# Optimization experiments

Measured on AMD Instinct MI355X. Metric: run time of the kernel, lower is better.

## Reference

```python
import jax
import jax.numpy as jnp
from jax import lax
import numpy as np

B, T, IN, H, K = 8, 4096, 512, 512, 2


def setup_inputs() -> dict:
    key = jax.random.key(0)
    k = jax.random.split(key, 5)
    scale_w0 = 1.0 / np.sqrt(IN * K)
    scale_w1 = 1.0 / np.sqrt(H * K)
    return {
        "x": jax.random.normal(k[0], (B, T, IN), jnp.float32),
        "w0": jax.random.normal(k[1], (3 * H, IN, K), jnp.float32) * scale_w0,
        "b0": jax.random.normal(k[2], (3 * H,), jnp.float32) * scale_w0,
        "w1": jax.random.normal(k[3], (3 * H, H, K), jnp.float32) * scale_w1,
        "b1": jax.random.normal(k[4], (3 * H,), jnp.float32) * scale_w1,
    }


def _qrnn_layer(x, w, b):
    # x: [B, T, C]; w: [3H, C, K]; causal conv (left pad K-1), matching
    # torch padding=K-1 then slicing off the last K-1 timesteps.
    xc = jnp.transpose(x, (0, 2, 1))  # [B, C, T]
    conv = lax.conv_general_dilated(
        xc, w, window_strides=(1,), padding=[(K - 1, 0)],
        dimension_numbers=("NCH", "OIH", "NCH"))
    conv = conv + b[None, :, None]
    conv = jnp.transpose(conv, (0, 2, 1))  # [B, T, 3H]
    z, f, o = jnp.split(conv, 3, axis=-1)
    z = jnp.tanh(z)
    f = jax.nn.sigmoid(f)
    o = jax.nn.sigmoid(o)

    def step(h, zfo):
        zt, ft, ot = zfo
        h = ft * h + (1.0 - ft) * zt  # fo-pool recurrence
        return h, ot * h

    h0 = jnp.zeros((x.shape[0], z.shape[-1]), x.dtype)
    hT, outs = lax.scan(
        step, h0,
        (jnp.swapaxes(z, 0, 1), jnp.swapaxes(f, 0, 1), jnp.swapaxes(o, 0, 1)))
    return jnp.swapaxes(outs, 0, 1), hT  # [B, T, H], [B, H]


def reference(x, w0, b0, w1, b1):
    out, h0 = _qrnn_layer(x, w0, b0)
    out, h1 = _qrnn_layer(out, w1, b1)
    return out, h0, h1
```

## Files before the change

### kernel.cpp

```cpp
#include <hip/hip_runtime.h>
#include <cstdint>

#define B_ 8
#define T_ 4096
#define TP1 4097
#define IN_ 512
#define H_ 512
#define N3H 1536
#define KD 1024
#define CHUNKS 128
#define CLEN 32

typedef __attribute__((ext_vector_type(4))) float floatx4;
typedef __attribute__((ext_vector_type(4))) float f4;
typedef __attribute__((ext_vector_type(8))) short short8;
typedef __attribute__((ext_vector_type(4))) unsigned short us4;
typedef __attribute__((ext_vector_type(4))) _Float16 h4;

__device__ __forceinline__ unsigned short f2bf(float v){
  unsigned int u = __float_as_uint(v);
  unsigned int r = (u + 0x7fffu + ((u >> 16) & 1u)) >> 16;
  return (unsigned short)r;
}
__device__ __forceinline__ float sigm(float x){ return 1.f/(1.f + __expf(-x)); }
__device__ __forceinline__ float tanhf_(float x){ return 2.f*sigm(2.f*x) - 1.f; }

#define GLLS(src, dst) __builtin_amdgcn_global_load_lds( \
    (const __attribute__((address_space(1))) void*)(src), \
    (__attribute__((address_space(3))) void*)(dst), 16, 0, 0)

__global__ void cast_pad_kernel(const float* __restrict__ x, unsigned short* __restrict__ xpad){
  int64_t i = (int64_t)blockIdx.x*256 + threadIdx.x;
  const int64_t total = (int64_t)B_*TP1*(IN_/4);
  if (i >= total) return;
  int cg = (int)(i & 127);
  int64_t r = i >> 7;
  int t = (int)(r % TP1);
  int b = (int)(r / TP1);
  us4 o;
  if (t == 0){ o = (us4){0,0,0,0}; }
  else {
    f4 v = *(const f4*)(x + ((int64_t)b*T_ + (t-1))*IN_ + cg*4);
    #pragma unroll
    for (int u=0;u<4;++u) o[u] = f2bf(v[u]);
  }
  *(us4*)(xpad + r*IN_ + cg*4) = o;
}

__global__ void wt_kernel(const float* __restrict__ wA, unsigned short* __restrict__ wtA,
                          const float* __restrict__ wB, unsigned short* __restrict__ wtB){
  int i = blockIdx.x*256 + threadIdx.x;
  if (i >= N3H*512) return;
  const float* w = blockIdx.y ? wB : wA;
  unsigned short* wt = blockIdx.y ? wtB : wtA;
  int ci = i & 511;
  int o = i >> 9;
  const float* wp = w + (int64_t)o*KD + ci*2;
  wt[(int64_t)o*KD + ci]       = f2bf(wp[0]);
  wt[(int64_t)o*KD + 512 + ci] = f2bf(wp[1]);
}

__global__ __launch_bounds__(256) void gemm_kernel(
    const unsigned short* __restrict__ A, const unsigned short* __restrict__ W,
    const float* __restrict__ bias, _Float16* __restrict__ C){
  __shared__ unsigned short As[2][128*32];
  __shared__ unsigned short Bs[2][128*32];
  const int tid = threadIdx.x;
  const int lane = tid & 63;
  const int wave = tid >> 6;
  const int bid = blockIdx.x;
  const int xcd = bid & 7;
  const int kb  = bid >> 3;
  const int colt = kb % 12;
  const int rowt = (kb / 12) * 8 + xcd;
  const int m0 = rowt * 128;
  const int n0 = colt * 128;
  const int bb = m0 / T_;
  const int act = n0 >> 9;
  const unsigned short* aSrc = A + (int64_t)(m0 + bb + (tid>>2))*IN_ + (tid&3)*8;
  const unsigned short* bSrc = W + (int64_t)(n0 + (tid>>2))*KD + (tid&3)*8;
  unsigned short* aDst0 = As[0] + tid*8;
  unsigned short* aDst1 = As[1] + tid*8;
  unsigned short* bDst0 = Bs[0] + tid*8;
  unsigned short* bDst1 = Bs[1] + tid*8;
  const int wm = wave & 1;
  const int wn = wave >> 1;
  const int l16 = lane & 15;
  const int quad = lane >> 4;
  floatx4 acc[4][4];
  #pragma unroll
  for (int i=0;i<4;i++)
    #pragma unroll
    for (int j=0;j<4;j++) acc[i][j] = (floatx4){0.f,0.f,0.f,0.f};
  const int fragOff = (wm*64 + l16)*32 + quad*8;
  const int fragOffB = (wn*64 + l16)*32 + quad*8;

  for (int kk = 0; kk < KD; kk += 64){
    __syncthreads();
    GLLS(aSrc + kk,             aDst0);
    GLLS(aSrc + 64*IN_ + kk,    aDst0 + 2048);
    GLLS(aSrc + kk + 32,        aDst1);
    GLLS(aSrc + 64*IN_ + kk+32, aDst1 + 2048);
    GLLS(bSrc + kk,             bDst0);
    GLLS(bSrc + 64*KD + kk,     bDst0 + 2048);
    GLLS(bSrc + kk + 32,        bDst1);
    GLLS(bSrc + 64*KD + kk+32,  bDst1 + 2048);
    __syncthreads();
    #pragma unroll
    for (int s=0;s<2;++s){
      const unsigned short* aLds = As[s] + fragOff;
      const unsigned short* bLds = Bs[s] + fragOffB;
      short8 af[4], bfr[4];
      #pragma unroll
      for (int i=0;i<4;i++) af[i] = *(const short8*)(aLds + i*16*32);
      #pragma unroll
      for (int j=0;j<4;j++) bfr[j] = *(const short8*)(bLds + j*16*32);
      #pragma unroll
      for (int i=0;i<4;i++)
        #pragma unroll
        for (int j=0;j<4;j++)
          acc[i][j] = __builtin_amdgcn_mfma_f32_16x16x32_bf16(af[i], bfr[j], acc[i][j], 0, 0, 0);
    }
  }
  float bv[4];
  #pragma unroll
  for (int j=0;j<4;j++) bv[j] = bias[n0 + wn*64 + j*16 + l16];
  #pragma unroll
  for (int i=0;i<4;i++){
    int row = m0 + wm*64 + i*16 + quad*4;
    #pragma unroll
    for (int j=0;j<4;j++){
      int col = n0 + wn*64 + j*16 + l16;
      _Float16* cp = C + (int64_t)row*N3H + col;
      #pragma unroll
      for (int r=0;r<4;r++){
        float v = acc[i][j][r] + bv[j];
        v = (act == 0) ? tanhf_(v) : sigm(v);
        cp[(int64_t)r*N3H] = (_Float16)v;
      }
    }
  }
}

__global__ void scan_phase1(const _Float16* __restrict__ conv,
                            float* __restrict__ carA, float* __restrict__ carB){
  int q = blockIdx.x*256 + threadIdx.x;
  int chg = q & 127;
  int bq = (q >> 7) & 7;
  int c  = q >> 10;
  int ch = chg*4;
  f4 Aa = {1.f,1.f,1.f,1.f}, Bb = {0.f,0.f,0.f,0.f};
  const _Float16* p = conv + ((int64_t)bq*T_ + c*CLEN)*N3H + ch;
  for (int g=0; g<CLEN/8; ++g){
    h4 zb[8], fb[8];
    #pragma unroll
    for (int u=0;u<8;++u){
      zb[u] = *(const h4*)(p + (int64_t)u*N3H);
      fb[u] = *(const h4*)(p + (int64_t)u*N3H + 512);
    }
    #pragma unroll
    for (int u=0;u<8;++u){
      #pragma unroll
      for (int v=0;v<4;++v){
        float fv = (float)fb[u][v];
        float zv = (float)zb[u][v];
        Aa[v] *= fv;
        Bb[v] = fv*Bb[v] + (1.f-fv)*zv;
      }
    }
    p += (int64_t)8*N3H;
  }
  *(f4*)(carA + (int64_t)q*4) = Aa;
  *(f4*)(carB + (int64_t)q*4) = Bb;
}

__global__ void scan_phase2(const float* __restrict__ carA, const float* __restrict__ carB,
                            float* __restrict__ hstart, float* __restrict__ hT){
  int q = blockIdx.x*256 + threadIdx.x;
  f4 h = {0.f,0.f,0.f,0.f};
  for (int g=0; g<CHUNKS/8; ++g){
    f4 av[8], bv[8];
    #pragma unroll
    for (int u=0;u<8;++u){
      int64_t idx = (int64_t)(g*8+u)*4096 + q*4;
      av[u] = *(const f4*)(carA + idx);
      bv[u] = *(const f4*)(carB + idx);
    }
    #pragma unroll
    for (int u=0;u<8;++u){
      int64_t idx = (int64_t)(g*8+u)*4096 + q*4;
      *(f4*)(hstart + idx) = h;
      #pragma unroll
      for (int v=0;v<4;++v) h[v] = av[u][v]*h[v] + bv[u][v];
    }
  }
  *(f4*)(hT + (int64_t)q*4) = h;
}

template<int LAYER>
__global__ void scan_phase3(const _Float16* __restrict__ conv,
                            const float* __restrict__ hstart, unsigned short* __restrict__ xpad,
                            float* __restrict__ outf){
  int q = blockIdx.x*256 + threadIdx.x;
  int chg = q & 127;
  int bq = (q >> 7) & 7;
  int c  = q >> 10;
  int ch = chg*4;
  f4 h = *(const f4*)(hstart + (int64_t)q*4);
  const _Float16* p = conv + ((int64_t)bq*T_ + c*CLEN)*N3H + ch;
  int t = c*CLEN;
  for (int g=0; g<CLEN/8; ++g){
    h4 zb[8], fb[8], ob[8];
    #pragma unroll
    for (int u=0;u<8;++u){
      zb[u] = *(const h4*)(p + (int64_t)u*N3H);
      fb[u] = *(const h4*)(p + (int64_t)u*N3H + 512);
      ob[u] = *(const h4*)(p + (int64_t)u*N3H + 1024);
    }
    #pragma unroll
    for (int u=0;u<8;++u){
      if (LAYER == 0){
        us4 ov4;
        #pragma unroll
        for (int v=0;v<4;++v){
          float fv = (float)fb[u][v];
          h[v] = fv*h[v] + (1.f-fv)*(float)zb[u][v];
          ov4[v] = f2bf((float)ob[u][v]*h[v]);
        }
        *(us4*)(xpad + ((int64_t)bq*TP1 + t+u + 1)*IN_ + ch) = ov4;
      } else {
        f4 of4;
        #pragma unroll
        for (int v=0;v<4;++v){
          float fv = (float)fb[u][v];
          h[v] = fv*h[v] + (1.f-fv)*(float)zb[u][v];
          of4[v] = (float)ob[u][v]*h[v];
        }
        *(f4*)(outf + ((int64_t)bq*T_ + t+u)*H_ + ch) = of4;
      }
    }
    t += 8; p += (int64_t)8*N3H;
  }
}

extern "C" void kernel_launch(void* const* d_in, const int* in_sizes, int n_in,
                              void* d_out, int out_size, void* d_ws, size_t ws_size,
                              hipStream_t stream){
  const float* x  = (const float*)d_in[0];
  const float* w0 = (const float*)d_in[1];
  const float* b0 = (const float*)d_in[2];
  const float* w1 = (const float*)d_in[3];
  const float* b1 = (const float*)d_in[4];
  float* out = (float*)d_out;

  char* ws = (char*)d_ws;
  size_t off = 0;
  auto alloc = [&](size_t bytes)->char*{
    char* p = ws + off; off = (off + bytes + 255) & ~(size_t)255; return p; };
  unsigned short* xpad = (unsigned short*)alloc((size_t)B_*TP1*IN_*2);
  unsigned short* Wt0  = (unsigned short*)alloc((size_t)N3H*KD*2);
  unsigned short* Wt1  = (unsigned short*)alloc((size_t)N3H*KD*2);
  _Float16* conv = (_Float16*)alloc((size_t)B_*T_*N3H*2);
  float* carA = (float*)alloc((size_t)CHUNKS*4096*4);
  float* carB = (float*)alloc((size_t)CHUNKS*4096*4);
  float* hst  = (float*)alloc((size_t)CHUNKS*4096*4);
  if (off > ws_size) return;

  float* out_main = out;
  float* h0 = out + (int64_t)B_*T_*H_;
  float* h1 = h0 + B_*H_;

  const int64_t padN = (int64_t)B_*TP1*(IN_/4);
  cast_pad_kernel<<<(int)((padN + 255)/256), 256, 0, stream>>>(x, xpad);
  dim3 wgrid((N3H*512 + 255)/256, 2);
  wt_kernel<<<wgrid, 256, 0, stream>>>(w0, Wt0, w1, Wt1);

  const int ggrid = (N3H/128) * ((B_*T_)/128);
  const int sgrid = (CHUNKS*8*128) / 256;
  gemm_kernel<<<ggrid, 256, 0, stream>>>(xpad, Wt0, b0, conv);
  scan_phase1<<<sgrid, 256, 0, stream>>>(conv, carA, carB);
  scan_phase2<<<4, 256, 0, stream>>>(carA, carB, hst, h0);
  scan_phase3<0><<<sgrid, 256, 0, stream>>>(conv, hst, xpad, nullptr);

  gemm_kernel<<<ggrid, 256, 0, stream>>>(xpad, Wt1, b1, conv);
  scan_phase1<<<sgrid, 256, 0, stream>>>(conv, carA, carB);
  scan_phase2<<<4, 256, 0, stream>>>(carA, carB, hst, h1);
  scan_phase3<1><<<sgrid, 256, 0, stream>>>(conv, hst, nullptr, out_main);
}
```

Baseline: 499.3 us.

## Move bias and gate activations into scan kernels, shrink GEMM K-step and scan chunks

The GEMM epilogue no longer adds bias or applies tanh/sigmoid and stores raw pre-activations in fp16. Bias and activations are now computed in scan phase 1 and phase 3, so z and f activations run twice. The GEMM K loop now stages 32 instead of 64 per sync, and the scan uses 256 chunks of 16 instead of 128 of 32. This trades GEMM epilogue work and LDS use for more synchronisation, duplicated transcendentals and a longer serial phase 2. Storing pre-activations rather than activations in fp16 also changes rounding.

```diff
diff --git a/kernel.cpp b/kernel.cpp
--- a/kernel.cpp
+++ b/kernel.cpp
@@ -8,8 +8,8 @@
 #define H_ 512
 #define N3H 1536
 #define KD 1024
-#define CHUNKS 128
-#define CLEN 32
+#define CHUNKS 256
+#define CLEN 16
 
 typedef __attribute__((ext_vector_type(4))) float floatx4;
 typedef __attribute__((ext_vector_type(4))) float f4;
@@ -62,9 +62,9 @@
 
 __global__ __launch_bounds__(256) void gemm_kernel(
     const unsigned short* __restrict__ A, const unsigned short* __restrict__ W,
-    const float* __restrict__ bias, _Float16* __restrict__ C){
-  __shared__ unsigned short As[2][128*32];
-  __shared__ unsigned short Bs[2][128*32];
+    _Float16* __restrict__ C){
+  __shared__ unsigned short As[128*32];
+  __shared__ unsigned short Bs[128*32];
   const int tid = threadIdx.x;
   const int lane = tid & 63;
   const int wave = tid >> 6;
@@ -76,13 +76,10 @@
   const int m0 = rowt * 128;
   const int n0 = colt * 128;
   const int bb = m0 / T_;
-  const int act = n0 >> 9;
   const unsigned short* aSrc = A + (int64_t)(m0 + bb + (tid>>2))*IN_ + (tid&3)*8;
   const unsigned short* bSrc = W + (int64_t)(n0 + (tid>>2))*KD + (tid&3)*8;
-  unsigned short* aDst0 = As[0] + tid*8;
-  unsigned short* aDst1 = As[1] + tid*8;
-  unsigned short* bDst0 = Bs[0] + tid*8;
-  unsigned short* bDst1 = Bs[1] + tid*8;
+  unsigned short* aDst = As + tid*8;
+  unsigned short* bDst = Bs + tid*8;
   const int wm = wave & 1;
   const int wn = wave >> 1;
   const int l16 = lane & 15;
@@ -92,39 +89,27 @@
   for (int i=0;i<4;i++)
     #pragma unroll
     for (int j=0;j<4;j++) acc[i][j] = (floatx4){0.f,0.f,0.f,0.f};
-  const int fragOff = (wm*64 + l16)*32 + quad*8;
-  const int fragOffB = (wn*64 + l16)*32 + quad*8;
-
-  for (int kk = 0; kk < KD; kk += 64){
+  const unsigned short* aLds = As + (wm*64 + l16)*32 + quad*8;
+  const unsigned short* bLds = Bs + (wn*64 + l16)*32 + quad*8;
+
+  for (int kk = 0; kk < KD; kk += 32){
     __syncthreads();
-    GLLS(aSrc + kk,             aDst0);
-    GLLS(aSrc + 64*IN_ + kk,    aDst0 + 2048);
-    GLLS(aSrc + kk + 32,        aDst1);
-    GLLS(aSrc + 64*IN_ + kk+32, aDst1 + 2048);
-    GLLS(bSrc + kk,             bDst0);
-    GLLS(bSrc + 64*KD + kk,     bDst0 + 2048);
-    GLLS(bSrc + kk + 32,        bDst1);
-    GLLS(bSrc + 64*KD + kk+32,  bDst1 + 2048);
+    GLLS(aSrc + kk,           aDst);
+    GLLS(aSrc + 64*IN_ + kk,  aDst + 2048);
+    GLLS(bSrc + kk,           bDst);
+    GLLS(bSrc + 64*KD + kk,   bDst + 2048);
     __syncthreads();
-    #pragma unroll
-    for (int s=0;s<2;++s){
-      const unsigned short* aLds = As[s] + fragOff;
-      const unsigned short* bLds = Bs[s] + fragOffB;
-      short8 af[4], bfr[4];
-      #pragma unroll
-      for (int i=0;i<4;i++) af[i] = *(const short8*)(aLds + i*16*32);
-      #pragma unroll
-      for (int j=0;j<4;j++) bfr[j] = *(const short8*)(bLds + j*16*32);
-      #pragma unroll
-      for (int i=0;i<4;i++)
-        #pragma unroll
-        for (int j=0;j<4;j++)
-          acc[i][j] = __builtin_amdgcn_mfma_f32_16x16x32_bf16(af[i], bfr[j], acc[i][j], 0, 0, 0);
-    }
-  }
-  float bv[4];
-  #pragma unroll
-  for (int j=0;j<4;j++) bv[j] = bias[n0 + wn*64 + j*16 + l16];
+    short8 af[4], bfr[4];
+    #pragma unroll
+    for (int i=0;i<4;i++) af[i] = *(const short8*)(aLds + i*16*32);
+    #pragma unroll
+    for (int j=0;j<4;j++) bfr[j] = *(const short8*)(bLds + j*16*32);
+    #pragma unroll
+    for (int i=0;i<4;i++)
+      #pragma unroll
+      for (int j=0;j<4;j++)
+        acc[i][j] = __builtin_amdgcn_mfma_f32_16x16x32_bf16(af[i], bfr[j], acc[i][j], 0, 0, 0);
+  }
   #pragma unroll
   for (int i=0;i<4;i++){
     int row = m0 + wm*64 + i*16 + quad*4;
@@ -133,22 +118,20 @@
       int col = n0 + wn*64 + j*16 + l16;
       _Float16* cp = C + (int64_t)row*N3H + col;
       #pragma unroll
-      for (int r=0;r<4;r++){
-        float v = acc[i][j][r] + bv[j];
-        v = (act == 0) ? tanhf_(v) : sigm(v);
-        cp[(int64_t)r*N3H] = (_Float16)v;
-      }
-    }
-  }
-}
-
-__global__ void scan_phase1(const _Float16* __restrict__ conv,
+      for (int r=0;r<4;r++) cp[(int64_t)r*N3H] = (_Float16)acc[i][j][r];
+    }
+  }
+}
+
+__global__ void scan_phase1(const _Float16* __restrict__ conv, const float* __restrict__ bias,
                             float* __restrict__ carA, float* __restrict__ carB){
   int q = blockIdx.x*256 + threadIdx.x;
   int chg = q & 127;
   int bq = (q >> 7) & 7;
   int c  = q >> 10;
   int ch = chg*4;
+  f4 bz = *(const f4*)(bias + ch);
+  f4 bf = *(const f4*)(bias + 512 + ch);
   f4 Aa = {1.f,1.f,1.f,1.f}, Bb = {0.f,0.f,0.f,0.f};
   const _Float16* p = conv + ((int64_t)bq*T_ + c*CLEN)*N3H + ch;
   for (int g=0; g<CLEN/8; ++g){
@@ -162,8 +145,8 @@
     for (int u=0;u<8;++u){
       #pragma unroll
       for (int v=0;v<4;++v){
-        float fv = (float)fb[u][v];
-        float zv = (float)zb[u][v];
+        float fv = sigm((float)fb[u][v] + bf[v]);
+        float zv = tanhf_((float)zb[u][v] + bz[v]);
         Aa[v] *= fv;
         Bb[v] = fv*Bb[v] + (1.f-fv)*zv;
       }
@@ -198,7 +181,7 @@
 }
 
 template<int LAYER>
-__global__ void scan_phase3(const _Float16* __restrict__ conv,
+__global__ void scan_phase3(const _Float16* __restrict__ conv, const float* __restrict__ bias,
                             const float* __restrict__ hstart, unsigned short* __restrict__ xpad,
                             float* __restrict__ outf){
   int q = blockIdx.x*256 + threadIdx.x;
@@ -206,6 +189,9 @@
   int bq = (q >> 7) & 7;
   int c  = q >> 10;
   int ch = chg*4;
+  f4 bz = *(const f4*)(bias + ch);
+  f4 bf = *(const f4*)(bias + 512 + ch);
+  f4 bo = *(const f4*)(bias + 1024 + ch);
   f4 h = *(const f4*)(hstart + (int64_t)q*4);
   const _Float16* p = conv + ((int64_t)bq*T_ + c*CLEN)*N3H + ch;
   int t = c*CLEN;
@@ -223,18 +209,22 @@
         us4 ov4;
         #pragma unroll
         for (int v=0;v<4;++v){
-          float fv = (float)fb[u][v];
-          h[v] = fv*h[v] + (1.f-fv)*(float)zb[u][v];
-          ov4[v] = f2bf((float)ob[u][v]*h[v]);
+          float fv = sigm((float)fb[u][v] + bf[v]);
+          float zv = tanhf_((float)zb[u][v] + bz[v]);
+          float ov = sigm((float)ob[u][v] + bo[v]);
+          h[v] = fv*h[v] + (1.f-fv)*zv;
+          ov4[v] = f2bf(ov*h[v]);
         }
         *(us4*)(xpad + ((int64_t)bq*TP1 + t+u + 1)*IN_ + ch) = ov4;
       } else {
         f4 of4;
         #pragma unroll
         for (int v=0;v<4;++v){
-          float fv = (float)fb[u][v];
-          h[v] = fv*h[v] + (1.f-fv)*(float)zb[u][v];
-          of4[v] = (float)ob[u][v]*h[v];
+          float fv = sigm((float)fb[u][v] + bf[v]);
+          float zv = tanhf_((float)zb[u][v] + bz[v]);
+          float ov = sigm((float)ob[u][v] + bo[v]);
+          h[v] = fv*h[v] + (1.f-fv)*zv;
+          of4[v] = ov*h[v];
         }
         *(f4*)(outf + ((int64_t)bq*T_ + t+u)*H_ + ch) = of4;
       }
@@ -277,13 +267,13 @@
 
   const int ggrid = (N3H/128) * ((B_*T_)/128);
   const int sgrid = (CHUNKS*8*128) / 256;
-  gemm_kernel<<<ggrid, 256, 0, stream>>>(xpad, Wt0, b0, conv);
-  scan_phase1<<<sgrid, 256, 0, stream>>>(conv, carA, carB);
+  gemm_kernel<<<ggrid, 256, 0, stream>>>(xpad, Wt0, conv);
+  scan_phase1<<<sgrid, 256, 0, stream>>>(conv, b0, carA, carB);
   scan_phase2<<<4, 256, 0, stream>>>(carA, carB, hst, h0);
-  scan_phase3<0><<<sgrid, 256, 0, stream>>>(conv, hst, xpad, nullptr);
-
-  gemm_kernel<<<ggrid, 256, 0, stream>>>(xpad, Wt1, b1, conv);
-  scan_phase1<<<sgrid, 256, 0, stream>>>(conv, carA, carB);
+  scan_phase3<0><<<sgrid, 256, 0, stream>>>(conv, b0, hst, xpad, nullptr);
+
+  gemm_kernel<<<ggrid, 256, 0, stream>>>(xpad, Wt1, conv);
+  scan_phase1<<<sgrid, 256, 0, stream>>>(conv, b1, carA, carB);
   scan_phase2<<<4, 256, 0, stream>>>(carA, carB, hst, h1);
-  scan_phase3<1><<<sgrid, 256, 0, stream>>>(conv, hst, nullptr, out_main);
-}
+  scan_phase3<1><<<sgrid, 256, 0, stream>>>(conv, b1, hst, nullptr, out_main);
+}
```

After: 531.0 us. 6.4% more time.

## Halve scan chunk count, shrink GEMM K-step, use rcp sigmoid, widen phase2 grid

Applied to the files above, without the earlier changes.

Several unrelated changes land together. The chunked scan now uses 64 chunks of length 64 instead of 128 of length 32. The GEMM loads a single 32-wide K slice per barrier instead of two, halving LDS use but doubling the number of sync points. Sigmoid uses the hardware reciprocal builtin, and scan_phase2 runs one scalar channel per thread across 16 blocks instead of float4 per thread across 4 blocks. Fewer chunks mean less parallelism in phases 1 and 3, and the extra GEMM barriers may cost more than the occupancy gained from the smaller LDS footprint.

```diff
diff --git a/kernel.cpp b/kernel.cpp
--- a/kernel.cpp
+++ b/kernel.cpp
@@ -8,8 +8,8 @@
 #define H_ 512
 #define N3H 1536
 #define KD 1024
-#define CHUNKS 128
-#define CLEN 32
+#define CHUNKS 64
+#define CLEN 64
 
 typedef __attribute__((ext_vector_type(4))) float floatx4;
 typedef __attribute__((ext_vector_type(4))) float f4;
@@ -22,7 +22,9 @@
   unsigned int r = (u + 0x7fffu + ((u >> 16) & 1u)) >> 16;
   return (unsigned short)r;
 }
-__device__ __forceinline__ float sigm(float x){ return 1.f/(1.f + __expf(-x)); }
+__device__ __forceinline__ float sigm(float x){
+  return __builtin_amdgcn_rcpf(1.f + __expf(-x));
+}
 __device__ __forceinline__ float tanhf_(float x){ return 2.f*sigm(2.f*x) - 1.f; }
 
 #define GLLS(src, dst) __builtin_amdgcn_global_load_lds( \
@@ -63,8 +65,8 @@
 __global__ __launch_bounds__(256) void gemm_kernel(
     const unsigned short* __restrict__ A, const unsigned short* __restrict__ W,
     const float* __restrict__ bias, _Float16* __restrict__ C){
-  __shared__ unsigned short As[2][128*32];
-  __shared__ unsigned short Bs[2][128*32];
+  __shared__ unsigned short As[128*32];
+  __shared__ unsigned short Bs[128*32];
   const int tid = threadIdx.x;
   const int lane = tid & 63;
   const int wave = tid >> 6;
@@ -79,10 +81,8 @@
   const int act = n0 >> 9;
   const unsigned short* aSrc = A + (int64_t)(m0 + bb + (tid>>2))*IN_ + (tid&3)*8;
   const unsigned short* bSrc = W + (int64_t)(n0 + (tid>>2))*KD + (tid&3)*8;
-  unsigned short* aDst0 = As[0] + tid*8;
-  unsigned short* aDst1 = As[1] + tid*8;
-  unsigned short* bDst0 = Bs[0] + tid*8;
-  unsigned short* bDst1 = Bs[1] + tid*8;
+  unsigned short* aDst = As + tid*8;
+  unsigned short* bDst = Bs + tid*8;
   const int wm = wave & 1;
   const int wn = wave >> 1;
   const int l16 = lane & 15;
@@ -92,35 +92,26 @@
   for (int i=0;i<4;i++)
     #pragma unroll
     for (int j=0;j<4;j++) acc[i][j] = (floatx4){0.f,0.f,0.f,0.f};
-  const int fragOff = (wm*64 + l16)*32 + quad*8;
-  const int fragOffB = (wn*64 + l16)*32 + quad*8;
-
-  for (int kk = 0; kk < KD; kk += 64){
+  const unsigned short* aLds = As + (wm*64 + l16)*32 + quad*8;
+  const unsigned short* bLds = Bs + (wn*64 + l16)*32 + quad*8;
+
+  for (int kk = 0; kk < KD; kk += 32){
     __syncthreads();
-    GLLS(aSrc + kk,             aDst0);
-    GLLS(aSrc + 64*IN_ + kk,    aDst0 + 2048);
-    GLLS(aSrc + kk + 32,        aDst1);
-    GLLS(aSrc + 64*IN_ + kk+32, aDst1 + 2048);
-    GLLS(bSrc + kk,             bDst0);
-    GLLS(bSrc + 64*KD + kk,     bDst0 + 2048);
-    GLLS(bSrc + kk + 32,        bDst1);
-    GLLS(bSrc + 64*KD + kk+32,  bDst1 + 2048);
+    GLLS(aSrc + kk,           aDst);
+    GLLS(aSrc + 64*IN_ + kk,  aDst + 2048);
+    GLLS(bSrc + kk,           bDst);
+    GLLS(bSrc + 64*KD + kk,   bDst + 2048);
     __syncthreads();
-    #pragma unroll
-    for (int s=0;s<2;++s){
-      const unsigned short* aLds = As[s] + fragOff;
-      const unsigned short* bLds = Bs[s] + fragOffB;
-      short8 af[4], bfr[4];
+    short8 af[4], bfr[4];
+    #pragma unroll
+    for (int i=0;i<4;i++) af[i] = *(const short8*)(aLds + i*16*32);
+    #pragma unroll
+    for (int j=0;j<4;j++) bfr[j] = *(const short8*)(bLds + j*16*32);
+    #pragma unroll
+    for (int i=0;i<4;i++)
       #pragma unroll
-      for (int i=0;i<4;i++) af[i] = *(const short8*)(aLds + i*16*32);
-      #pragma unroll
-      for (int j=0;j<4;j++) bfr[j] = *(const short8*)(bLds + j*16*32);
-      #pragma unroll
-      for (int i=0;i<4;i++)
-        #pragma unroll
-        for (int j=0;j<4;j++)
-          acc[i][j] = __builtin_amdgcn_mfma_f32_16x16x32_bf16(af[i], bfr[j], acc[i][j], 0, 0, 0);
-    }
+      for (int j=0;j<4;j++)
+        acc[i][j] = __builtin_amdgcn_mfma_f32_16x16x32_bf16(af[i], bfr[j], acc[i][j], 0, 0, 0);
   }
   float bv[4];
   #pragma unroll
@@ -177,24 +168,13 @@
 __global__ void scan_phase2(const float* __restrict__ carA, const float* __restrict__ carB,
                             float* __restrict__ hstart, float* __restrict__ hT){
   int q = blockIdx.x*256 + threadIdx.x;
-  f4 h = {0.f,0.f,0.f,0.f};
-  for (int g=0; g<CHUNKS/8; ++g){
-    f4 av[8], bv[8];
-    #pragma unroll
-    for (int u=0;u<8;++u){
-      int64_t idx = (int64_t)(g*8+u)*4096 + q*4;
-      av[u] = *(const f4*)(carA + idx);
-      bv[u] = *(const f4*)(carB + idx);
-    }
-    #pragma unroll
-    for (int u=0;u<8;++u){
-      int64_t idx = (int64_t)(g*8+u)*4096 + q*4;
-      *(f4*)(hstart + idx) = h;
-      #pragma unroll
-      for (int v=0;v<4;++v) h[v] = av[u][v]*h[v] + bv[u][v];
-    }
-  }
-  *(f4*)(hT + (int64_t)q*4) = h;
+  float h = 0.f;
+  for (int c=0;c<CHUNKS;++c){
+    int64_t idx = (int64_t)c*4096 + q;
+    hstart[idx] = h;
+    h = carA[idx]*h + carB[idx];
+  }
+  hT[q] = h;
 }
 
 template<int LAYER>
@@ -206,7 +186,9 @@
   int bq = (q >> 7) & 7;
   int c  = q >> 10;
   int ch = chg*4;
-  f4 h = *(const f4*)(hstart + (int64_t)q*4);
+  f4 h;
+  #pragma unroll
+  for (int v=0;v<4;++v) h[v] = hstart[(int64_t)c*4096 + bq*512 + ch + v];
   const _Float16* p = conv + ((int64_t)bq*T_ + c*CLEN)*N3H + ch;
   int t = c*CLEN;
   for (int g=0; g<CLEN/8; ++g){
@@ -279,11 +261,11 @@
   const int sgrid = (CHUNKS*8*128) / 256;
   gemm_kernel<<<ggrid, 256, 0, stream>>>(xpad, Wt0, b0, conv);
   scan_phase1<<<sgrid, 256, 0, stream>>>(conv, carA, carB);
-  scan_phase2<<<4, 256, 0, stream>>>(carA, carB, hst, h0);
+  scan_phase2<<<16, 256, 0, stream>>>(carA, carB, hst, h0);
   scan_phase3<0><<<sgrid, 256, 0, stream>>>(conv, hst, xpad, nullptr);
 
   gemm_kernel<<<ggrid, 256, 0, stream>>>(xpad, Wt1, b1, conv);
   scan_phase1<<<sgrid, 256, 0, stream>>>(conv, carA, carB);
-  scan_phase2<<<4, 256, 0, stream>>>(carA, carB, hst, h1);
+  scan_phase2<<<16, 256, 0, stream>>>(carA, carB, hst, h1);
   scan_phase3<1><<<sgrid, 256, 0, stream>>>(conv, hst, nullptr, out_main);
 }
```

After: 458.0 us. 8.3% less time.
